# Kernel tuning notes

Hardware: AMD Instinct MI355X
Metric: run time of the kernel (lower is better)

Reference implementation:

```python
import jax, jax.numpy as jnp
import numpy as np

G, N, D, E, L, OUT = 64, 1024, 128, 16384, 2, 64


def setup_inputs() -> dict:
    key = jax.random.key(0)
    ks = jax.random.split(key, 7)
    input_feature = jax.random.normal(ks[0], (G, N, D), jnp.float32)
    edge_index = jax.random.randint(ks[1], (G, 2, E), 0, N, jnp.int32)
    # GraphConv(D, 1): lin_rel (with bias) applied to aggregated neighbors, lin_root (no bias)
    w_rel = jax.random.normal(ks[2], (L, D), jnp.float32) / np.sqrt(D).astype(np.float32)
    b_rel = jnp.zeros((L,), jnp.float32)
    w_root = jax.random.normal(ks[3], (L, D), jnp.float32) / np.sqrt(D).astype(np.float32)
    # SelectTopK(1, ratio): weight is a [1,1] scalar per layer
    w_sel = jax.random.normal(ks[4], (L,), jnp.float32) + 1.5  # keep away from 0
    W_lin = jax.random.normal(ks[5], (2 * D, OUT), jnp.float32) / np.sqrt(2 * D).astype(np.float32)
    b_lin = jnp.zeros((OUT,), jnp.float32)
    return dict(input_feature=input_feature, edge_index=edge_index, w_rel=w_rel,
                b_rel=b_rel, w_root=w_root, w_sel=w_sel, W_lin=W_lin, b_lin=b_lin)


def _sagpool(x, ei, emask, w_rel, b_rel, w_root, w_sel):
    # x: [g, n, d]; ei: [g, 2, e]; emask: [g, e] bool (invalid edges contribute zero)
    g, n, d = x.shape
    src, dst = ei[:, 0], ei[:, 1]  # [g, e] (source_to_target flow)
    gidx = jnp.arange(g)[:, None]
    # GraphConv attention score (out_channels = 1)
    msg = jnp.take_along_axis(x, src[..., None], axis=1) * emask[..., None].astype(x.dtype)  # [g,e,d]
    agg = jnp.zeros_like(x).at[gidx, dst].add(msg)  # segment-sum over dst, [g,n,d]
    attn = agg @ w_rel + b_rel + x @ w_root  # [g, n]
    # SelectTopK: score = tanh(attn * w / ||w||), then per-graph top-k (k = n//2 since ratio=0.5)
    score = jnp.tanh(attn * (w_sel / jnp.abs(w_sel)))
    k = n // 2
    top_s, perm = jax.lax.top_k(score, k)  # [g, k]
    new_x = jnp.take_along_axis(x, perm[..., None], axis=1) * top_s[..., None]  # [g, k, d]
    # FilterEdges: keep edges with both endpoints selected, remap to new node ids
    new_idx = jnp.full((g, n), -1, jnp.int32).at[gidx, perm].set(
        jnp.broadcast_to(jnp.arange(k, dtype=jnp.int32)[None, :], (g, k)))
    src2 = jnp.take_along_axis(new_idx, src, axis=1)
    dst2 = jnp.take_along_axis(new_idx, dst, axis=1)
    new_mask = emask & (src2 >= 0) & (dst2 >= 0)
    src2 = jnp.where(new_mask, src2, 0)
    dst2 = jnp.where(new_mask, dst2, 0)
    return new_x, jnp.stack([src2, dst2], axis=1), new_mask


def reference(input_feature, edge_index, w_rel, b_rel, w_root, w_sel, W_lin, b_lin):
    x, ei = input_feature, edge_index
    emask = jnp.ones((ei.shape[0], ei.shape[2]), dtype=bool)
    for l in range(L):
        x, ei, emask = _sagpool(x, ei, emask, w_rel[l], b_rel[l], w_root[l], w_sel[l])
    # global_mean_pool || global_max_pool per graph, then Linear(2D -> OUT)
    readout = jnp.concatenate([x.mean(axis=1), x.max(axis=1)], axis=-1)  # [G, 2D]
    return readout @ W_lin + b_lin
```

## Files before the change

kernel.cpp:

```cpp
#include <hip/hip_runtime.h>
#include <stdint.h>

#define NG   64
#define N0   1024
#define N1   512
#define DD   128
#define NE   16384
#define NOUT 64

__device__ __forceinline__ float waveReduceSum(float v) {
    for (int off = 32; off > 0; off >>= 1) v += __shfl_xor(v, off, 64);
    return v;
}

__global__ __launch_bounds__(256) void dots1_kernel(
    const float* __restrict__ x,
    const float* __restrict__ w_rel, const float* __restrict__ w_root,
    const float* __restrict__ b_rel_p,
    float* __restrict__ s_rel, float* __restrict__ attn,
    int totalNodes)
{
    int wave = blockIdx.x * 4 + (threadIdx.x >> 6);
    int lane = threadIdx.x & 63;
    float wr0 = w_rel[lane * 2],  wr1 = w_rel[lane * 2 + 1];
    float wo0 = w_root[lane * 2], wo1 = w_root[lane * 2 + 1];
    float brel = *b_rel_p;
    #pragma unroll
    for (int t = 0; t < 4; ++t) {
        int node = wave * 4 + t;
        if (node >= totalNodes) return;
        const float2 v = *(const float2*)(x + (size_t)node * DD + lane * 2);
        float pr = waveReduceSum(v.x * wr0 + v.y * wr1);
        float po = waveReduceSum(v.x * wo0 + v.y * wo1);
        if (lane == 0) { s_rel[node] = pr; attn[node] = po + brel; }
    }
}

__global__ __launch_bounds__(256) void scatter1_kernel(
    const int* __restrict__ ei,
    const float* __restrict__ s_rel,
    float* __restrict__ attn)
{
    int e = blockIdx.x * 256 + threadIdx.x;
    int g = e >> 14, eo = e & (NE - 1);
    const int* base = ei + (size_t)g * 2 * NE;
    int s = base[eo], d = base[NE + eo];
    atomicAdd(&attn[(g << 10) + d], s_rel[(g << 10) + s]);
}

template<int NN, int KK>
__global__ __launch_bounds__(NN) void topk_kernel(
    const float* __restrict__ attn,
    const float* __restrict__ w_sel_p,
    int*   __restrict__ permOut,
    float* __restrict__ topsOut,
    int*   __restrict__ newidxOut)
{
    __shared__ unsigned long long lds[NN];
    const int g = blockIdx.x, i = threadIdx.x;
    const float sgn = (*w_sel_p >= 0.f) ? 1.f : -1.f;

    float sc = tanhf(attn[(size_t)g * NN + i] * sgn);
    unsigned int u = __float_as_uint(sc);
    u = (u & 0x80000000u) ? ~u : (u | 0x80000000u);
    unsigned long long key =
        ((unsigned long long)u << 32) | (unsigned int)(NN - 1 - i);

    for (int k2 = 2; k2 <= NN; k2 <<= 1) {
        for (int j = k2 >> 1; j > 0; j >>= 1) {
            unsigned long long p;
            if (j >= 64) {
                __syncthreads();
                lds[i] = key;
                __syncthreads();
                p = lds[i ^ j];
            } else {
                p = __shfl_xor(key, j, 64);
            }
            bool keepMax = (((i & k2) == 0) == ((i & j) == 0));
            if (keepMax ? (p > key) : (p < key)) key = p;
        }
    }

    int idx = (NN - 1) - (int)(key & 0xffffffffu);
    unsigned int ku = (unsigned int)(key >> 32);
    unsigned int fb = (ku & 0x80000000u) ? (ku ^ 0x80000000u) : ~ku;
    if (i < KK) {
        permOut[(size_t)g * KK + i] = idx;
        topsOut[(size_t)g * KK + i] = __uint_as_float(fb);
    }
    if (newidxOut) newidxOut[(size_t)g * NN + idx] = (i < KK) ? i : -1;
}

__global__ __launch_bounds__(256) void gdots2_kernel(
    const float* __restrict__ x0,
    const int*   __restrict__ perm1,
    const float* __restrict__ tops1,
    const float* __restrict__ w_rel, const float* __restrict__ w_root,
    const float* __restrict__ b_rel_p,
    float* __restrict__ s_rel2, float* __restrict__ attn2,
    int totalOut)
{
    int wave = blockIdx.x * 4 + (threadIdx.x >> 6);
    int lane = threadIdx.x & 63;
    float wr0 = w_rel[lane * 2],  wr1 = w_rel[lane * 2 + 1];
    float wo0 = w_root[lane * 2], wo1 = w_root[lane * 2 + 1];
    float brel = *b_rel_p;
    #pragma unroll
    for (int t = 0; t < 4; ++t) {
        int j = wave * 4 + t;
        if (j >= totalOut) return;
        int g = j >> 9;
        int node = perm1[j];
        float scl = tops1[j];
        const float2 v = *(const float2*)(x0 + ((size_t)(g << 10) + node) * DD + lane * 2);
        float pr = waveReduceSum(v.x * wr0 + v.y * wr1);
        float po = waveReduceSum(v.x * wo0 + v.y * wo1);
        if (lane == 0) { s_rel2[j] = scl * pr; attn2[j] = scl * po + brel; }
    }
}

__global__ __launch_bounds__(256) void remap_scatter2_kernel(
    const int* __restrict__ ei,
    const int* __restrict__ newidx1,
    const float* __restrict__ s_rel2,
    float* __restrict__ attn2)
{
    int e = blockIdx.x * 256 + threadIdx.x;
    int g = e >> 14, eo = e & (NE - 1);
    const int* base = ei + (size_t)g * 2 * NE;
    int s = base[eo], d = base[NE + eo];
    int s2 = newidx1[(g << 10) + s];
    int d2 = newidx1[(g << 10) + d];
    if ((s2 | d2) >= 0)
        atomicAdd(&attn2[(g << 9) + d2], s_rel2[(g << 9) + s2]);
}

__global__ __launch_bounds__(512) void readout_kernel(
    const float* __restrict__ x0,
    const int*   __restrict__ perm1,
    const float* __restrict__ tops1,
    const int*   __restrict__ perm2,
    const float* __restrict__ tops2,
    const float* __restrict__ W_lin,
    const float* __restrict__ b_lin,
    float* __restrict__ out)
{
    __shared__ float sm[4][DD], mm[4][DD], r[2 * DD];
    __shared__ float po[4][NOUT];
    const int g = blockIdx.x, tid = threadIdx.x;
    const int d = tid & (DD - 1), q = tid >> 7;
    const int*   p2 = perm2 + (size_t)g * 256;
    const float* t2 = tops2 + (size_t)g * 256;
    const int*   p1 = perm1 + (size_t)g * N1;
    const float* t1 = tops1 + (size_t)g * N1;

    float sum = 0.f, mx = -3.0e38f;
    #pragma unroll 4
    for (int j = q * 64; j < q * 64 + 64; ++j) {
        int r1 = p2[j];
        float sc = t2[j] * t1[r1];
        int n0 = p1[r1];
        float v = x0[((size_t)(g << 10) + n0) * DD + d] * sc;
        sum += v;
        mx = fmaxf(mx, v);
    }
    sm[q][d] = sum; mm[q][d] = mx;
    __syncthreads();
    if (tid < DD) {
        r[tid] = (sm[0][tid] + sm[1][tid] + sm[2][tid] + sm[3][tid]) * (1.f / 256.f);
    } else if (tid < 2 * DD) {
        int dd = tid - DD;
        r[DD + dd] = fmaxf(fmaxf(mm[0][dd], mm[1][dd]), fmaxf(mm[2][dd], mm[3][dd]));
    }
    __syncthreads();
    if (tid < 256) {
        int o = tid & (NOUT - 1), c = tid >> 6;
        float acc = 0.f;
        #pragma unroll
        for (int i2 = 0; i2 < 64; ++i2) {
            int i = c * 64 + i2;
            acc += r[i] * W_lin[i * NOUT + o];
        }
        po[c][o] = acc;
    }
    __syncthreads();
    if (tid < NOUT)
        out[(size_t)g * NOUT + tid] =
            b_lin[tid] + po[0][tid] + po[1][tid] + po[2][tid] + po[3][tid];
}

extern "C" void kernel_launch(void* const* d_in, const int* in_sizes, int n_in,
                              void* d_out, int out_size, void* d_ws, size_t ws_size,
                              hipStream_t stream)
{
    const float* x0     = (const float*)d_in[0];
    const int*   ei     = (const int*)  d_in[1];
    const float* w_rel  = (const float*)d_in[2];
    const float* b_rel  = (const float*)d_in[3];
    const float* w_root = (const float*)d_in[4];
    const float* w_sel  = (const float*)d_in[5];
    const float* W_lin  = (const float*)d_in[6];
    const float* b_lin  = (const float*)d_in[7];
    float* out = (float*)d_out;
    (void)in_sizes; (void)n_in; (void)out_size; (void)ws_size;

    char* ws = (char*)d_ws;
    size_t off = 0;
    auto alloc = [&](size_t bytes) -> void* {
        off = (off + 255) & ~(size_t)255;
        void* p = ws + off;
        off += bytes;
        return p;
    };

    float* s_rel1  = (float*)alloc((size_t)NG * N0 * 4);
    float* attn1   = (float*)alloc((size_t)NG * N0 * 4);
    int*   perm1   = (int*)  alloc((size_t)NG * N1 * 4);
    float* tops1   = (float*)alloc((size_t)NG * N1 * 4);
    int*   newidx1 = (int*)  alloc((size_t)NG * N0 * 4);
    float* s_rel2  = (float*)alloc((size_t)NG * N1 * 4);
    float* attn2   = (float*)alloc((size_t)NG * N1 * 4);
    int*   perm2   = (int*)  alloc((size_t)NG * 256 * 4);
    float* tops2   = (float*)alloc((size_t)NG * 256 * 4);

    dots1_kernel<<<(NG * N0) / 16, 256, 0, stream>>>(
        x0, w_rel, w_root, b_rel, s_rel1, attn1, NG * N0);

    scatter1_kernel<<<(NG * NE) / 256, 256, 0, stream>>>(ei, s_rel1, attn1);

    topk_kernel<N0, N1><<<NG, N0, 0, stream>>>(
        attn1, w_sel, perm1, tops1, newidx1);

    gdots2_kernel<<<(NG * N1) / 16, 256, 0, stream>>>(
        x0, perm1, tops1, w_rel + DD, w_root + DD, b_rel + 1,
        s_rel2, attn2, NG * N1);

    remap_scatter2_kernel<<<(NG * NE) / 256, 256, 0, stream>>>(
        ei, newidx1, s_rel2, attn2);

    topk_kernel<N1, 256><<<NG, N1, 0, stream>>>(
        attn2, w_sel + 1, perm2, tops2, nullptr);

    readout_kernel<<<NG, 512, 0, stream>>>(
        x0, perm1, tops1, perm2, tops2, W_lin, b_lin, out);
}
```

Measured before the change: 193.8 us.

## Fuse edge scatter and top-k into per-graph kernels with LDS atomics

Per-graph blocks now do the edge scatter-add with shared-memory atomics, reading edges as int4. Each block then runs the bitonic top-k in place, so the separate scatter and top-k kernels are merged. The second layer also folds its scatter, top-k and readout into one kernel, so perm2/tops2 never go through global memory. This cuts launch count and global atomic traffic, but the scatter now runs on only 64 blocks, one per graph, which lowers parallelism.

Result: faster. 162.3 us (-16.3%).

```diff
diff --git a/kernel.cpp b/kernel.cpp
--- a/kernel.cpp
+++ b/kernel.cpp
@@ -4,6 +4,7 @@
 #define NG   64
 #define N0   1024
 #define N1   512
+#define K2   256
 #define DD   128
 #define NE   16384
 #define NOUT 64
@@ -13,59 +14,10 @@
     return v;
 }
 
-__global__ __launch_bounds__(256) void dots1_kernel(
-    const float* __restrict__ x,
-    const float* __restrict__ w_rel, const float* __restrict__ w_root,
-    const float* __restrict__ b_rel_p,
-    float* __restrict__ s_rel, float* __restrict__ attn,
-    int totalNodes)
-{
-    int wave = blockIdx.x * 4 + (threadIdx.x >> 6);
-    int lane = threadIdx.x & 63;
-    float wr0 = w_rel[lane * 2],  wr1 = w_rel[lane * 2 + 1];
-    float wo0 = w_root[lane * 2], wo1 = w_root[lane * 2 + 1];
-    float brel = *b_rel_p;
-    #pragma unroll
-    for (int t = 0; t < 4; ++t) {
-        int node = wave * 4 + t;
-        if (node >= totalNodes) return;
-        const float2 v = *(const float2*)(x + (size_t)node * DD + lane * 2);
-        float pr = waveReduceSum(v.x * wr0 + v.y * wr1);
-        float po = waveReduceSum(v.x * wo0 + v.y * wo1);
-        if (lane == 0) { s_rel[node] = pr; attn[node] = po + brel; }
-    }
-}
-
-__global__ __launch_bounds__(256) void scatter1_kernel(
-    const int* __restrict__ ei,
-    const float* __restrict__ s_rel,
-    float* __restrict__ attn)
-{
-    int e = blockIdx.x * 256 + threadIdx.x;
-    int g = e >> 14, eo = e & (NE - 1);
-    const int* base = ei + (size_t)g * 2 * NE;
-    int s = base[eo], d = base[NE + eo];
-    atomicAdd(&attn[(g << 10) + d], s_rel[(g << 10) + s]);
-}
-
-template<int NN, int KK>
-__global__ __launch_bounds__(NN) void topk_kernel(
-    const float* __restrict__ attn,
-    const float* __restrict__ w_sel_p,
-    int*   __restrict__ permOut,
-    float* __restrict__ topsOut,
-    int*   __restrict__ newidxOut)
-{
-    __shared__ unsigned long long lds[NN];
-    const int g = blockIdx.x, i = threadIdx.x;
-    const float sgn = (*w_sel_p >= 0.f) ? 1.f : -1.f;
-
-    float sc = tanhf(attn[(size_t)g * NN + i] * sgn);
-    unsigned int u = __float_as_uint(sc);
-    u = (u & 0x80000000u) ? ~u : (u | 0x80000000u);
-    unsigned long long key =
-        ((unsigned long long)u << 32) | (unsigned int)(NN - 1 - i);
-
+template<int NN>
+__device__ __forceinline__ unsigned long long bitonic_desc(
+    unsigned long long key, unsigned long long* lds, int i)
+{
     for (int k2 = 2; k2 <= NN; k2 <<= 1) {
         for (int j = k2 >> 1; j > 0; j >>= 1) {
             unsigned long long p;
@@ -81,15 +33,82 @@
             if (keepMax ? (p > key) : (p < key)) key = p;
         }
     }
-
-    int idx = (NN - 1) - (int)(key & 0xffffffffu);
+    return key;
+}
+
+__device__ __forceinline__ unsigned long long make_key(float attnv, float sgn, int i, int nn) {
+    float sc = tanhf(attnv * sgn);
+    unsigned int u = __float_as_uint(sc);
+    u = (u & 0x80000000u) ? ~u : (u | 0x80000000u);
+    return ((unsigned long long)u << 32) | (unsigned int)(nn - 1 - i);
+}
+
+__global__ __launch_bounds__(256) void dots1_kernel(
+    const float* __restrict__ x,
+    const float* __restrict__ w_rel, const float* __restrict__ w_root,
+    const float* __restrict__ b_rel_p,
+    float* __restrict__ s_rel, float* __restrict__ attn,
+    int totalNodes)
+{
+    int wave = blockIdx.x * 4 + (threadIdx.x >> 6);
+    int lane = threadIdx.x & 63;
+    float wr0 = w_rel[lane * 2],  wr1 = w_rel[lane * 2 + 1];
+    float wo0 = w_root[lane * 2], wo1 = w_root[lane * 2 + 1];
+    float brel = *b_rel_p;
+    #pragma unroll
+    for (int t = 0; t < 4; ++t) {
+        int node = wave * 4 + t;
+        if (node >= totalNodes) return;
+        const float2 v = *(const float2*)(x + (size_t)node * DD + lane * 2);
+        float pr = waveReduceSum(v.x * wr0 + v.y * wr1);
+        float po = waveReduceSum(v.x * wo0 + v.y * wo1);
+        if (lane == 0) { s_rel[node] = pr; attn[node] = po + brel; }
+    }
+}
+
+__global__ __launch_bounds__(1024) void graph1_kernel(
+    const float* __restrict__ s_rel1,
+    const float* __restrict__ attn1in,
+    const float* __restrict__ w_sel_p,
+    const int*   __restrict__ ei,
+    int*   __restrict__ perm1,
+    float* __restrict__ tops1,
+    int*   __restrict__ newidx1)
+{
+    __shared__ float srel[N0];
+    __shared__ float attn[N0];
+    __shared__ unsigned long long keys[N0];
+    const int g = blockIdx.x, i = threadIdx.x;
+
+    srel[i] = s_rel1[(size_t)g * N0 + i];
+    attn[i] = attn1in[(size_t)g * N0 + i];
+    __syncthreads();
+
+    const int* base = ei + (size_t)g * 2 * NE;
+    #pragma unroll
+    for (int it = 0; it < 4; ++it) {
+        int eo = (it * 1024 + i) * 4;
+        const int4 s4 = *(const int4*)(base + eo);
+        const int4 d4 = *(const int4*)(base + NE + eo);
+        atomicAdd(&attn[d4.x], srel[s4.x]);
+        atomicAdd(&attn[d4.y], srel[s4.y]);
+        atomicAdd(&attn[d4.z], srel[s4.z]);
+        atomicAdd(&attn[d4.w], srel[s4.w]);
+    }
+    __syncthreads();
+
+    const float sgn = (*w_sel_p >= 0.f) ? 1.f : -1.f;
+    unsigned long long key = make_key(attn[i], sgn, i, N0);
+    key = bitonic_desc<N0>(key, keys, i);
+
+    int idx = (N0 - 1) - (int)(key & 0xffffffffu);
     unsigned int ku = (unsigned int)(key >> 32);
     unsigned int fb = (ku & 0x80000000u) ? (ku ^ 0x80000000u) : ~ku;
-    if (i < KK) {
-        permOut[(size_t)g * KK + i] = idx;
-        topsOut[(size_t)g * KK + i] = __uint_as_float(fb);
-    }
-    if (newidxOut) newidxOut[(size_t)g * NN + idx] = (i < KK) ? i : -1;
+    if (i < N1) {
+        perm1[(size_t)g * N1 + i] = idx;
+        tops1[(size_t)g * N1 + i] = __uint_as_float(fb);
+    }
+    newidx1[(size_t)g * N0 + idx] = (i < N1) ? i : -1;
 }
 
 __global__ __launch_bounds__(256) void gdots2_kernel(
@@ -120,74 +139,96 @@
     }
 }
 
-__global__ __launch_bounds__(256) void remap_scatter2_kernel(
-    const int* __restrict__ ei,
-    const int* __restrict__ newidx1,
-    const float* __restrict__ s_rel2,
-    float* __restrict__ attn2)
-{
-    int e = blockIdx.x * 256 + threadIdx.x;
-    int g = e >> 14, eo = e & (NE - 1);
-    const int* base = ei + (size_t)g * 2 * NE;
-    int s = base[eo], d = base[NE + eo];
-    int s2 = newidx1[(g << 10) + s];
-    int d2 = newidx1[(g << 10) + d];
-    if ((s2 | d2) >= 0)
-        atomicAdd(&attn2[(g << 9) + d2], s_rel2[(g << 9) + s2]);
-}
-
-__global__ __launch_bounds__(512) void readout_kernel(
+__global__ __launch_bounds__(512) void graph2_readout_kernel(
     const float* __restrict__ x0,
+    const int*   __restrict__ ei,
+    const int*   __restrict__ newidx1,
     const int*   __restrict__ perm1,
     const float* __restrict__ tops1,
-    const int*   __restrict__ perm2,
-    const float* __restrict__ tops2,
+    const float* __restrict__ s_rel2,
+    const float* __restrict__ attn2in,
+    const float* __restrict__ w_sel_p,
     const float* __restrict__ W_lin,
     const float* __restrict__ b_lin,
     float* __restrict__ out)
 {
-    __shared__ float sm[4][DD], mm[4][DD], r[2 * DD];
-    __shared__ float po[4][NOUT];
-    const int g = blockIdx.x, tid = threadIdx.x;
-    const int d = tid & (DD - 1), q = tid >> 7;
-    const int*   p2 = perm2 + (size_t)g * 256;
-    const float* t2 = tops2 + (size_t)g * 256;
-    const int*   p1 = perm1 + (size_t)g * N1;
-    const float* t1 = tops1 + (size_t)g * N1;
-
+    __shared__ int   nidx[N0];
+    __shared__ float srel[N1];
+    __shared__ float attn[N1];
+    __shared__ unsigned long long keys[N1];
+    __shared__ int   p1l[N1];
+    __shared__ float t1l[N1];
+    __shared__ int   cn0[K2];
+    __shared__ float cs[K2];
+    __shared__ float sm[4][DD], mm[4][DD], rr[2 * DD], po[4][NOUT];
+
+    const int g = blockIdx.x, i = threadIdx.x;
+    nidx[i]       = newidx1[(size_t)g * N0 + i];
+    nidx[i + 512] = newidx1[(size_t)g * N0 + i + 512];
+    srel[i] = s_rel2[(size_t)g * N1 + i];
+    attn[i] = attn2in[(size_t)g * N1 + i];
+    p1l[i]  = perm1[(size_t)g * N1 + i];
+    t1l[i]  = tops1[(size_t)g * N1 + i];
+    __syncthreads();
+
+    const int* base = ei + (size_t)g * 2 * NE;
+    #pragma unroll
+    for (int it = 0; it < 8; ++it) {
+        int eo = (it * 512 + i) * 4;
+        const int4 s4 = *(const int4*)(base + eo);
+        const int4 d4 = *(const int4*)(base + NE + eo);
+        int s2, d2;
+        s2 = nidx[s4.x]; d2 = nidx[d4.x]; if ((s2 | d2) >= 0) atomicAdd(&attn[d2], srel[s2]);
+        s2 = nidx[s4.y]; d2 = nidx[d4.y]; if ((s2 | d2) >= 0) atomicAdd(&attn[d2], srel[s2]);
+        s2 = nidx[s4.z]; d2 = nidx[d4.z]; if ((s2 | d2) >= 0) atomicAdd(&attn[d2], srel[s2]);
+        s2 = nidx[s4.w]; d2 = nidx[d4.w]; if ((s2 | d2) >= 0) atomicAdd(&attn[d2], srel[s2]);
+    }
+    __syncthreads();
+
+    const float sgn = (*w_sel_p >= 0.f) ? 1.f : -1.f;
+    unsigned long long key = make_key(attn[i], sgn, i, N1);
+    key = bitonic_desc<N1>(key, keys, i);
+
+    int idx = (N1 - 1) - (int)(key & 0xffffffffu);
+    unsigned int ku = (unsigned int)(key >> 32);
+    unsigned int fb = (ku & 0x80000000u) ? (ku ^ 0x80000000u) : ~ku;
+    if (i < K2) {
+        cn0[i] = p1l[idx];
+        cs[i]  = __uint_as_float(fb) * t1l[idx];
+    }
+    __syncthreads();
+
+    const int d = i & (DD - 1), q = i >> 7;
     float sum = 0.f, mx = -3.0e38f;
     #pragma unroll 4
     for (int j = q * 64; j < q * 64 + 64; ++j) {
-        int r1 = p2[j];
-        float sc = t2[j] * t1[r1];
-        int n0 = p1[r1];
-        float v = x0[((size_t)(g << 10) + n0) * DD + d] * sc;
+        float v = x0[((size_t)(g << 10) + cn0[j]) * DD + d] * cs[j];
         sum += v;
         mx = fmaxf(mx, v);
     }
     sm[q][d] = sum; mm[q][d] = mx;
     __syncthreads();
-    if (tid < DD) {
-        r[tid] = (sm[0][tid] + sm[1][tid] + sm[2][tid] + sm[3][tid]) * (1.f / 256.f);
-    } else if (tid < 2 * DD) {
-        int dd = tid - DD;
-        r[DD + dd] = fmaxf(fmaxf(mm[0][dd], mm[1][dd]), fmaxf(mm[2][dd], mm[3][dd]));
-    }
-    __syncthreads();
-    if (tid < 256) {
-        int o = tid & (NOUT - 1), c = tid >> 6;
+    if (i < DD) {
+        rr[i] = (sm[0][i] + sm[1][i] + sm[2][i] + sm[3][i]) * (1.f / 256.f);
+    } else if (i < 2 * DD) {
+        int dd = i - DD;
+        rr[DD + dd] = fmaxf(fmaxf(mm[0][dd], mm[1][dd]), fmaxf(mm[2][dd], mm[3][dd]));
+    }
+    __syncthreads();
+    if (i < 256) {
+        int o = i & (NOUT - 1), c = i >> 6;
         float acc = 0.f;
         #pragma unroll
         for (int i2 = 0; i2 < 64; ++i2) {
-            int i = c * 64 + i2;
-            acc += r[i] * W_lin[i * NOUT + o];
+            int ii = c * 64 + i2;
+            acc += rr[ii] * W_lin[ii * NOUT + o];
         }
         po[c][o] = acc;
     }
     __syncthreads();
-    if (tid < NOUT)
-        out[(size_t)g * NOUT + tid] =
-            b_lin[tid] + po[0][tid] + po[1][tid] + po[2][tid] + po[3][tid];
+    if (i < NOUT)
+        out[(size_t)g * NOUT + i] =
+            b_lin[i] + po[0][i] + po[1][i] + po[2][i] + po[3][i];
 }
 
 extern "C" void kernel_launch(void* const* d_in, const int* in_sizes, int n_in,
@@ -221,27 +262,18 @@
     int*   newidx1 = (int*)  alloc((size_t)NG * N0 * 4);
     float* s_rel2  = (float*)alloc((size_t)NG * N1 * 4);
     float* attn2   = (float*)alloc((size_t)NG * N1 * 4);
-    int*   perm2   = (int*)  alloc((size_t)NG * 256 * 4);
-    float* tops2   = (float*)alloc((size_t)NG * 256 * 4);
 
     dots1_kernel<<<(NG * N0) / 16, 256, 0, stream>>>(
         x0, w_rel, w_root, b_rel, s_rel1, attn1, NG * N0);
 
-    scatter1_kernel<<<(NG * NE) / 256, 256, 0, stream>>>(ei, s_rel1, attn1);
-
-    topk_kernel<N0, N1><<<NG, N0, 0, stream>>>(
-        attn1, w_sel, perm1, tops1, newidx1);
+    graph1_kernel<<<NG, 1024, 0, stream>>>(
+        s_rel1, attn1, w_sel, ei, perm1, tops1, newidx1);
 
     gdots2_kernel<<<(NG * N1) / 16, 256, 0, stream>>>(
         x0, perm1, tops1, w_rel + DD, w_root + DD, b_rel + 1,
         s_rel2, attn2, NG * N1);
 
-    remap_scatter2_kernel<<<(NG * NE) / 256, 256, 0, stream>>>(
-        ei, newidx1, s_rel2, attn2);
-
-    topk_kernel<N1, 256><<<NG, N1, 0, stream>>>(
-        attn2, w_sel + 1, perm2, tops2, nullptr);
-
-    readout_kernel<<<NG, 512, 0, stream>>>(
-        x0, perm1, tops1, perm2, tops2, W_lin, b_lin, out);
-}
+    graph2_readout_kernel<<<NG, 512, 0, stream>>>(
+        x0, ei, newidx1, perm1, tops1, s_rel2, attn2, w_sel + 1,
+        W_lin, b_lin, out);
+}
```
